# Kernel tuning notes

Measured on AMD Instinct MI355X. Metric: run time of the kernel, lower is better.

## Reference

```python
import jax, jax.numpy as jnp
import numpy as np

B, F, U, A, H = 8192, 1024, 256, 16, 8  # batch, in_features, units_layer, num_actions, hidden(=8)


def _coagent_layer(x, W0, b0, W1, b1, W2, b2):
    # x: [B, f_in]; stacked weights for U independent tiny MLPs (grouped GEMMs)
    h = jax.nn.relu(jnp.einsum('bf,uhf->buh', x, W0) + b0)   # [B, U, H]
    h = jax.nn.relu(jnp.einsum('buh,ugh->bug', h, W1) + b1)  # [B, U, H]
    q = jnp.einsum('bug,uag->bua', h, W2) + b2               # [B, U, A]
    # greedy action per coagent (epsilon-greedy with greedy=True / epsilon=0)
    return jnp.argmax(q, axis=-1).astype(jnp.float32)        # [B, U]


def setup_inputs() -> dict:
    key = jax.random.key(0)
    ks = jax.random.split(key, 19)
    n = lambda k, shape, fan: (jax.random.normal(k, shape, dtype=jnp.float32)
                               / jnp.sqrt(jnp.float32(fan)))
    return {
        'state': jax.random.normal(ks[0], (B, F), dtype=jnp.float32),
        # coagent layer 0: in_features -> 8 -> 8 -> A, stacked over U units
        'W0_0': n(ks[1], (U, H, F), F), 'b0_0': jnp.zeros((U, H), jnp.float32),
        'W1_0': n(ks[2], (U, H, H), H), 'b1_0': jnp.zeros((U, H), jnp.float32),
        'W2_0': n(ks[3], (U, A, H), H), 'b2_0': jnp.zeros((U, A), jnp.float32),
        # coagent layer 1: units_layer -> 8 -> 8 -> A, stacked over U units
        'W0_1': n(ks[4], (U, H, U), U), 'b0_1': jnp.zeros((U, H), jnp.float32),
        'W1_1': n(ks[5], (U, H, H), H), 'b1_1': jnp.zeros((U, H), jnp.float32),
        'W2_1': n(ks[6], (U, A, H), H), 'b2_1': jnp.zeros((U, A), jnp.float32),
        # Policy head: units_layer -> 8 -> 8 -> 1
        'PW0': n(ks[7], (H, U), U), 'Pb0': jnp.zeros((H,), jnp.float32),
        'PW1': n(ks[8], (H, H), H), 'Pb1': jnp.zeros((H,), jnp.float32),
        'PW2': n(ks[9], (1, H), H), 'Pb2': jnp.zeros((1,), jnp.float32),
    }


def reference(state, W0_0, b0_0, W1_0, b1_0, W2_0, b2_0,
              W0_1, b0_1, W1_1, b1_1, W2_1, b2_1,
              PW0, Pb0, PW1, Pb1, PW2, Pb2):
    a0 = _coagent_layer(state, W0_0, b0_0, W1_0, b1_0, W2_0, b2_0)  # [B, U]
    a1 = _coagent_layer(a0, W0_1, b0_1, W1_1, b1_1, W2_1, b2_1)     # [B, U]
    h = jax.nn.relu(a1 @ PW0.T + Pb0)
    h = jax.nn.relu(h @ PW1.T + Pb1)
    return h @ PW2.T + Pb2  # [B, 1]
```

## Files before the change

kernel.cpp:

```cpp
#include <hip/hip_runtime.h>
#include <cstring>
#include <cstdint>

#define B_TOTAL 8192
#define F_IN    1024
#define U_UNITS 256
#define NACT    16
#define HID     8

typedef float    f32x4  __attribute__((ext_vector_type(4)));
typedef _Float16 half8  __attribute__((ext_vector_type(8)));


__device__ __forceinline__ void gload_lds16(const _Float16* g, _Float16* l)
{
    __builtin_amdgcn_global_load_lds(
        (const __attribute__((address_space(1))) void*)g,
        (__attribute__((address_space(3))) void*)l,
        16, 0, 0);
}

__global__ __launch_bounds__(256)
void pack3_kernel(const float* __restrict__ s0, _Float16* __restrict__ d0h, _Float16* __restrict__ d0l,
                  const float* __restrict__ s1, _Float16* __restrict__ d1h, _Float16* __restrict__ d1l,
                  const float* __restrict__ s2, _Float16* __restrict__ d2h, _Float16* __restrict__ d2l)
{
    constexpr int NB0 = (B_TOTAL / 16) * (F_IN / 128);
    constexpr int NB1 = (U_UNITS * HID / 16) * (F_IN / 128);
    __shared__ float ls[16 * 132];
    int b = blockIdx.x;
    const float* src; _Float16 *dh, *dl; int K, lg;
    if (b < NB0)            { src = s0; dh = d0h; dl = d0l; K = F_IN;    lg = 3; }
    else if (b < NB0 + NB1) { b -= NB0; src = s1; dh = d1h; dl = d1l; K = F_IN; lg = 3; }
    else                    { b -= NB0 + NB1; src = s2; dh = d2h; dl = d2l; K = U_UNITS; lg = 1; }

    const int tid = threadIdx.x;
    const int mt  = b >> lg;
    const int kb  = b & ((1 << lg) - 1);
    const int r0  = mt * 16;

#pragma unroll
    for (int i = 0; i < 2; ++i) {
        const int e = tid + (i << 8);
        const int row = e >> 5;
        const int c4  = e & 31;
        f32x4 v = *reinterpret_cast<const f32x4*>(
            &src[(size_t)(r0 + row) * K + (kb << 7) + (c4 << 2)]);
        *reinterpret_cast<f32x4*>(&ls[row * 132 + (c4 << 2)]) = v;
    }
    __syncthreads();

    const int k8 = tid >> 4, r = tid & 15;
    float x[8];
#pragma unroll
    for (int j = 0; j < 8; ++j) x[j] = ls[r * 132 + (k8 << 3) + j];
    half8 h, l;
#pragma unroll
    for (int j = 0; j < 8; ++j) {
        h[j] = (_Float16)x[j];
        l[j] = (_Float16)((x[j] - (float)h[j]) * 2048.0f);
    }
    const size_t off = (((size_t)mt * (K >> 5)) + (kb << 2) + (k8 >> 2)) * 512
                     + (size_t)(((k8 & 3) << 4) + r) * 8;
    *reinterpret_cast<half8*>(&dh[off]) = h;
    *reinterpret_cast<half8*>(&dl[off]) = l;
}

constexpr int BM = 128, BN = 64;

template<int K_TOTAL, bool A_SPLIT, bool OUT_TF32>
__global__ __launch_bounds__(256, 4)
void coagent_mfma(const _Float16* __restrict__ Ahg, const _Float16* __restrict__ Alg,
                  const _Float16* __restrict__ Bhg, const _Float16* __restrict__ Blg,
                  const float* __restrict__ b0, const float* __restrict__ W1,
                  const float* __restrict__ b1, const float* __restrict__ W2,
                  const float* __restrict__ b2, void* __restrict__ outp)
{
    constexpr int BUFH  = A_SPLIT ? 12288 : 8192;
    constexpr int BOFFH = A_SPLIT ? 8192 : 4096;
    constexpr int BOFFL = A_SPLIT ? 10240 : 6144;
    constexpr int NCH   = A_SPLIT ? 6 : 4;

    struct EpiBufs { float Hs[BM][BN + 1]; _Float16 ab[BM * 8]; };
    union SMemU { _Float16 stage[2][BUFH]; EpiBufs epi; };
    __shared__ SMemU sm;

    constexpr int NTK = K_TOTAL >> 5;
    constexpr size_t TS = (size_t)NTK * 512;

    const int tid  = threadIdx.x;
    const int wave = tid >> 6;
    const int lane = tid & 63;
    const int quad = lane >> 4;
    const int l15  = lane & 15;

    const int m0 = blockIdx.y * BM;
    const int n0 = blockIdx.x * BN;

    const int wmi = wave >> 1, wni = wave & 1;
    const int at  = wmi * 4;
    const int bt  = wni * 2;
    const int wm  = wmi * 64, wn = wni * 32;

    const _Float16* gs[NCH];
#pragma unroll
    for (int i = 0; i < NCH; ++i) {
        const int c = wave * NCH + i;
        const _Float16* base; int tile;
        if (A_SPLIT) {
            if (c < 8)       { base = Ahg; tile = (m0 >> 4) + c; }
            else if (c < 16) { base = Alg; tile = (m0 >> 4) + (c - 8); }
            else if (c < 20) { base = Bhg; tile = (n0 >> 4) + (c - 16); }
            else             { base = Blg; tile = (n0 >> 4) + (c - 20); }
        } else {
            if (c < 8)       { base = Ahg; tile = (m0 >> 4) + c; }
            else if (c < 12) { base = Bhg; tile = (n0 >> 4) + (c - 8); }
            else             { base = Blg; tile = (n0 >> 4) + (c - 12); }
        }
        gs[i] = base + (size_t)tile * TS + lane * 8;
    }

    f32x4 acc1[4][2];
    f32x4 acc2[4][2];
#pragma unroll
    for (int i = 0; i < 4; ++i)
#pragma unroll
        for (int j = 0; j < 2; ++j) { acc1[i][j] = {0.f,0.f,0.f,0.f}; acc2[i][j] = {0.f,0.f,0.f,0.f}; }

#pragma unroll
    for (int i = 0; i < NCH; ++i)
        gload_lds16(gs[i], &sm.stage[0][(wave * NCH + i) * 512]);
    __syncthreads();

    int cur = 0;
#pragma unroll 1
    for (int kt = 0; kt < NTK; ++kt) {
        if (kt + 1 < NTK) {
            _Float16* nb = &sm.stage[cur ^ 1][0];
#pragma unroll
            for (int i = 0; i < NCH; ++i)
                gload_lds16(gs[i] + (size_t)(kt + 1) * 512, nb + (wave * NCH + i) * 512);
        }

        const _Float16* sb = &sm.stage[cur][0];
        half8 af[4], la[4];
#pragma unroll
        for (int mt = 0; mt < 4; ++mt)
            af[mt] = *reinterpret_cast<const half8*>(&sb[(at + mt) * 512 + lane * 8]);
        if constexpr (A_SPLIT) {
#pragma unroll
            for (int mt = 0; mt < 4; ++mt)
                la[mt] = *reinterpret_cast<const half8*>(&sb[4096 + (at + mt) * 512 + lane * 8]);
        }

#pragma unroll
        for (int nt = 0; nt < 2; ++nt) {
            half8 bf = *reinterpret_cast<const half8*>(&sb[BOFFH + (bt + nt) * 512 + lane * 8]);
            half8 lb = *reinterpret_cast<const half8*>(&sb[BOFFL + (bt + nt) * 512 + lane * 8]);
#pragma unroll
            for (int mt = 0; mt < 4; ++mt)
                acc1[mt][nt] = __builtin_amdgcn_mfma_f32_16x16x32_f16(af[mt], bf, acc1[mt][nt], 0, 0, 0);
            if constexpr (A_SPLIT) {
#pragma unroll
                for (int mt = 0; mt < 4; ++mt)
                    acc2[mt][nt] = __builtin_amdgcn_mfma_f32_16x16x32_f16(la[mt], bf, acc2[mt][nt], 0, 0, 0);
            }
#pragma unroll
            for (int mt = 0; mt < 4; ++mt)
                acc2[mt][nt] = __builtin_amdgcn_mfma_f32_16x16x32_f16(af[mt], lb, acc2[mt][nt], 0, 0, 0);
        }

        __syncthreads();
        cur ^= 1;
    }

#pragma unroll
    for (int mt = 0; mt < 4; ++mt)
#pragma unroll
        for (int nt = 0; nt < 2; ++nt)
#pragma unroll
            for (int r = 0; r < 4; ++r)
                sm.epi.Hs[wm + mt * 16 + quad * 4 + r][wn + nt * 16 + l15] =
                    acc1[mt][nt][r] + acc2[mt][nt][r] * (1.0f / 2048.0f);
    __syncthreads();

    const int ubase = n0 >> 3;
#pragma unroll
    for (int p = 0; p < 4; ++p) {
        const int idx = (p << 8) + tid;
        const int ul = idx >> 7;
        const int bl = idx & 127;
        const int u  = __builtin_amdgcn_readfirstlane(ubase + ul);
        const float* __restrict__ b0u = b0 + u * 8;
        const float* __restrict__ W1u = W1 + u * 64;
        const float* __restrict__ b1u = b1 + u * 8;
        const float* __restrict__ W2u = W2 + u * 128;
        const float* __restrict__ b2u = b2 + u * 16;

        float h[HID];
#pragma unroll
        for (int j = 0; j < HID; ++j)
            h[j] = fmaxf(sm.epi.Hs[bl][ul * 8 + j] + b0u[j], 0.f);

        float h2[HID];
#pragma unroll
        for (int g = 0; g < HID; ++g) {
            float s = b1u[g];
#pragma unroll
            for (int j = 0; j < HID; ++j)
                s += h[j] * W1u[g * 8 + j];
            h2[g] = fmaxf(s, 0.f);
        }

        float best = b2u[0];
#pragma unroll
        for (int j = 0; j < HID; ++j) best += h2[j] * W2u[j];
        int bi = 0;
#pragma unroll
        for (int a = 1; a < NACT; ++a) {
            float s = b2u[a];
#pragma unroll
            for (int j = 0; j < HID; ++j)
                s += h2[j] * W2u[a * 8 + j];
            if (s > best) { best = s; bi = a; }
        }

        if (OUT_TF32) {
            ((float*)outp)[(size_t)u * B_TOTAL + m0 + bl] = (float)bi;
        } else {
            sm.epi.ab[bl * 8 + ul] = (_Float16)bi;
        }
    }
    if (!OUT_TF32) {
        __syncthreads();
        if (tid < 128) {
            float4 v = *reinterpret_cast<float4*>(&sm.epi.ab[tid * 8]);
            const int u = ubase;
            const int b = m0 + tid;
            const size_t off = ((size_t)(b >> 4) * 8 + (u >> 5)) * 512
                             + (size_t)((((u >> 3) & 3) << 4) + (b & 15)) * 8;
            *reinterpret_cast<float4*>(&((_Float16*)outp)[off]) = v;
        }
    }
}


constexpr int FBM = 128, FBN = 128, FBK = 16;

template<int K_TOTAL, bool X_TRANSPOSED>
__global__ __launch_bounds__(256, 2)
void coagent_kernel(const float* __restrict__ X, const float* __restrict__ W0,
                    const float* __restrict__ b0, const float* __restrict__ W1,
                    const float* __restrict__ b1, const float* __restrict__ W2,
                    const float* __restrict__ b2, float* __restrict__ outT)
{
    struct SMemGemm { float As[FBK][FBM + 4]; float Bs[FBK][FBN + 4]; };
    union SMem { SMemGemm g; float Hs[FBM][65]; };
    __shared__ SMem sm;

    const int tid = threadIdx.x;
    const int tx = tid & 15, ty = tid >> 4;
    const int m0 = blockIdx.y * FBM, n0 = blockIdx.x * FBN;

    float acc[8][8];
#pragma unroll
    for (int i = 0; i < 8; ++i)
#pragma unroll
        for (int j = 0; j < 8; ++j) acc[i][j] = 0.f;

    for (int k0 = 0; k0 < K_TOTAL; k0 += FBK) {
        __syncthreads();
        if (X_TRANSPOSED) {
#pragma unroll
            for (int l = tid; l < (FBM * FBK) / 4; l += 256) {
                const int k = l >> 5, q = l & 31;
                const float4 v = *reinterpret_cast<const float4*>(
                    &X[(size_t)(k0 + k) * B_TOTAL + m0 + 4 * q]);
                *reinterpret_cast<float4*>(&sm.g.As[k][4 * q]) = v;
            }
        } else {
#pragma unroll
            for (int l = tid; l < (FBM * FBK) / 4; l += 256) {
                const int row = l >> 2, c = l & 3;
                const float4 v = *reinterpret_cast<const float4*>(
                    &X[(size_t)(m0 + row) * K_TOTAL + k0 + 4 * c]);
                sm.g.As[4 * c + 0][row] = v.x; sm.g.As[4 * c + 1][row] = v.y;
                sm.g.As[4 * c + 2][row] = v.z; sm.g.As[4 * c + 3][row] = v.w;
            }
        }
#pragma unroll
        for (int l = tid; l < (FBN * FBK) / 4; l += 256) {
            const int row = l >> 2, c = l & 3;
            const float4 v = *reinterpret_cast<const float4*>(
                &W0[(size_t)(n0 + row) * K_TOTAL + k0 + 4 * c]);
            sm.g.Bs[4 * c + 0][row] = v.x; sm.g.Bs[4 * c + 1][row] = v.y;
            sm.g.Bs[4 * c + 2][row] = v.z; sm.g.Bs[4 * c + 3][row] = v.w;
        }
        __syncthreads();
#pragma unroll
        for (int k = 0; k < FBK; ++k) {
            float a[8], bb[8];
            *reinterpret_cast<float4*>(&a[0])  = *reinterpret_cast<float4*>(&sm.g.As[k][4 * ty]);
            *reinterpret_cast<float4*>(&a[4])  = *reinterpret_cast<float4*>(&sm.g.As[k][64 + 4 * ty]);
            *reinterpret_cast<float4*>(&bb[0]) = *reinterpret_cast<float4*>(&sm.g.Bs[k][4 * tx]);
            *reinterpret_cast<float4*>(&bb[4]) = *reinterpret_cast<float4*>(&sm.g.Bs[k][64 + 4 * tx]);
#pragma unroll
            for (int i = 0; i < 8; ++i)
#pragma unroll
                for (int j = 0; j < 8; ++j) acc[i][j] += a[i] * bb[j];
        }
    }

    const int ub_base = n0 >> 3;
    for (int half = 0; half < 2; ++half) {
        __syncthreads();
#pragma unroll
        for (int i = 0; i < 8; ++i) {
            const int row = (i < 4) ? (4 * ty + i) : (64 + 4 * ty + (i - 4));
#pragma unroll
            for (int j = 0; j < 4; ++j)
                sm.Hs[row][4 * tx + j] = acc[i][4 * half + j];
        }
        __syncthreads();
#pragma unroll
        for (int p = 0; p < 4; ++p) {
            const int pair = (p << 8) + tid;
            const int ul = pair >> 7, bl = pair & 127;
            const int u = ub_base + half * 8 + ul;
            float h[HID];
#pragma unroll
            for (int j = 0; j < HID; ++j)
                h[j] = fmaxf(sm.Hs[bl][ul * 8 + j] + b0[u * 8 + j], 0.f);
            float h2[HID];
#pragma unroll
            for (int g = 0; g < HID; ++g) {
                float s = b1[u * 8 + g];
#pragma unroll
                for (int j = 0; j < HID; ++j) s += h[j] * W1[u * 64 + g * 8 + j];
                h2[g] = fmaxf(s, 0.f);
            }
            float best = b2[u * 16];
#pragma unroll
            for (int j = 0; j < HID; ++j) best += h2[j] * W2[u * 128 + j];
            int bi = 0;
#pragma unroll
            for (int a = 1; a < NACT; ++a) {
                float s = b2[u * 16 + a];
#pragma unroll
                for (int j = 0; j < HID; ++j) s += h2[j] * W2[u * 128 + a * 8 + j];
                if (s > best) { best = s; bi = a; }
            }
            outT[(size_t)u * B_TOTAL + m0 + bl] = (float)bi;
        }
    }
}

__global__ __launch_bounds__(256)
void policy_kernel(const float* __restrict__ A1T,
                   const float* __restrict__ PW0, const float* __restrict__ Pb0,
                   const float* __restrict__ PW1, const float* __restrict__ Pb1,
                   const float* __restrict__ PW2, const float* __restrict__ Pb2,
                   float* __restrict__ out)
{
    __shared__ float part[8][32][HID + 1];
    const int tid = threadIdx.x;
    const int b32 = tid & 31;
    const int sl  = tid >> 5;
    const int b   = blockIdx.x * 32 + b32;

    float hp[HID];
#pragma unroll
    for (int j = 0; j < HID; ++j) hp[j] = 0.f;

#pragma unroll 1
    for (int q0 = 0; q0 < 32; q0 += 8) {
        float v[8];
#pragma unroll
        for (int t = 0; t < 8; ++t)
            v[t] = A1T[(size_t)(sl * 32 + q0 + t) * B_TOTAL + b];
#pragma unroll
        for (int t = 0; t < 8; ++t)
#pragma unroll
            for (int j = 0; j < HID; ++j)
                hp[j] += v[t] * PW0[j * U_UNITS + sl * 32 + q0 + t];
    }
#pragma unroll
    for (int j = 0; j < HID; ++j) part[sl][b32][j] = hp[j];
    __syncthreads();

    if (sl == 0) {
        float h[HID];
#pragma unroll
        for (int j = 0; j < HID; ++j) {
            float s = Pb0[j];
#pragma unroll
            for (int s8 = 0; s8 < 8; ++s8) s += part[s8][b32][j];
            h[j] = fmaxf(s, 0.f);
        }
        float h2[HID];
#pragma unroll
        for (int g = 0; g < HID; ++g) {
            float s = Pb1[g];
#pragma unroll
            for (int j = 0; j < HID; ++j) s += h[j] * PW1[g * 8 + j];
            h2[g] = fmaxf(s, 0.f);
        }
        float o = Pb2[0];
#pragma unroll
        for (int j = 0; j < HID; ++j) o += h2[j] * PW2[j];
        out[b] = o;
    }
}


extern "C" void kernel_launch(void* const* d_in, const int* in_sizes, int n_in,
                              void* d_out, int out_size, void* d_ws, size_t ws_size,
                              hipStream_t stream)
{
    const float* state = (const float*)d_in[0];
    const float* W0_0  = (const float*)d_in[1];
    const float* b0_0  = (const float*)d_in[2];
    const float* W1_0  = (const float*)d_in[3];
    const float* b1_0  = (const float*)d_in[4];
    const float* W2_0  = (const float*)d_in[5];
    const float* b2_0  = (const float*)d_in[6];
    const float* W0_1  = (const float*)d_in[7];
    const float* b0_1  = (const float*)d_in[8];
    const float* W1_1  = (const float*)d_in[9];
    const float* b1_1  = (const float*)d_in[10];
    const float* W2_1  = (const float*)d_in[11];
    const float* b2_1  = (const float*)d_in[12];
    const float* PW0   = (const float*)d_in[13];
    const float* Pb0   = (const float*)d_in[14];
    const float* PW1   = (const float*)d_in[15];
    const float* Pb1   = (const float*)d_in[16];
    const float* PW2   = (const float*)d_in[17];
    const float* Pb2   = (const float*)d_in[18];

    const size_t SZ_STATE = (size_t)B_TOTAL * F_IN;
    const size_t SZ_W00   = (size_t)U_UNITS * HID * F_IN;
    const size_t SZ_W01   = (size_t)U_UNITS * HID * U_UNITS;
    const size_t NEED = (2 * SZ_STATE + 2 * SZ_W00 + 2 * SZ_W01
                         + (size_t)B_TOTAL * U_UNITS) * 2
                        + (size_t)U_UNITS * B_TOTAL * 4;

    if (ws_size >= NEED) {
        char* p = (char*)d_ws;
        _Float16* state_h = (_Float16*)p;                p += SZ_STATE * 2;
        _Float16* state_l = (_Float16*)p;                p += SZ_STATE * 2;
        _Float16* w00_h   = (_Float16*)p;                p += SZ_W00 * 2;
        _Float16* w00_l   = (_Float16*)p;                p += SZ_W00 * 2;
        _Float16* w01_h   = (_Float16*)p;                p += SZ_W01 * 2;
        _Float16* w01_l   = (_Float16*)p;                p += SZ_W01 * 2;
        _Float16* a0      = (_Float16*)p;                p += (size_t)B_TOTAL * U_UNITS * 2;
        float*    a1T     = (float*)p;

        constexpr int NB0 = (B_TOTAL / 16) * (F_IN / 128);
        constexpr int NB1 = (U_UNITS * HID / 16) * (F_IN / 128);
        constexpr int NB2 = (U_UNITS * HID / 16) * (U_UNITS / 128);
        pack3_kernel<<<NB0 + NB1 + NB2, 256, 0, stream>>>(
            state, state_h, state_l, W0_0, w00_h, w00_l, W0_1, w01_h, w01_l);

        dim3 grid((U_UNITS * HID) / BN, B_TOTAL / BM);

        coagent_mfma<F_IN, true, false><<<grid, 256, 0, stream>>>(
            state_h, state_l, w00_h, w00_l, b0_0, W1_0, b1_0, W2_0, b2_0, (void*)a0);

        coagent_mfma<U_UNITS, false, true><<<grid, 256, 0, stream>>>(
            a0, nullptr, w01_h, w01_l, b0_1, W1_1, b1_1, W2_1, b2_1, (void*)a1T);

        policy_kernel<<<B_TOTAL / 32, 256, 0, stream>>>(
            a1T, PW0, Pb0, PW1, Pb1, PW2, Pb2, (float*)d_out);
    } else {
        float* a0T = (float*)d_ws;
        float* a1T = a0T + (size_t)U_UNITS * B_TOTAL;
        dim3 grid((U_UNITS * HID) / FBN, B_TOTAL / FBM);
        coagent_kernel<F_IN, false><<<grid, 256, 0, stream>>>(
            state, W0_0, b0_0, W1_0, b1_0, W2_0, b2_0, a0T);
        coagent_kernel<U_UNITS, true><<<grid, 256, 0, stream>>>(
            a0T, W0_1, b0_1, W1_1, b1_1, W2_1, b2_1, a1T);
        policy_kernel<<<B_TOTAL / 32, 256, 0, stream>>>(
            a1T, PW0, Pb0, PW1, Pb1, PW2, Pb2, (float*)d_out);
    }
}
```

Baseline: 281.9 us.

## Triple-buffer LDS staging with prefetch distance two and explicit vmcnt waits

The K loop moves from double to triple buffering in LDS. Global-to-LDS loads are now issued two tiles ahead, and explicit s_waitcnt vmcnt counts wait only for the current tile, so one raw barrier per iteration replaces the trailing __syncthreads. The goal is to hide more global load latency behind the MFMA work and cut barrier stalls. In exchange, LDS use grows and the launch bounds lower the blocks-per-CU target to 2 or 3, which trades occupancy for deeper in-flight prefetch.

```diff
diff --git a/kernel.cpp b/kernel.cpp
--- a/kernel.cpp
+++ b/kernel.cpp
@@ -69,7 +69,7 @@
 constexpr int BM = 128, BN = 64;
 
 template<int K_TOTAL, bool A_SPLIT, bool OUT_TF32>
-__global__ __launch_bounds__(256, 4)
+__global__ __launch_bounds__(256, A_SPLIT ? 2 : 3)
 void coagent_mfma(const _Float16* __restrict__ Ahg, const _Float16* __restrict__ Alg,
                   const _Float16* __restrict__ Bhg, const _Float16* __restrict__ Blg,
                   const float* __restrict__ b0, const float* __restrict__ W1,
@@ -82,7 +82,7 @@
     constexpr int NCH   = A_SPLIT ? 6 : 4;
 
     struct EpiBufs { float Hs[BM][BN + 1]; _Float16 ab[BM * 8]; };
-    union SMemU { _Float16 stage[2][BUFH]; EpiBufs epi; };
+    union SMemU { _Float16 stage[3][BUFH]; EpiBufs epi; };
     __shared__ SMemU sm;
 
     constexpr int NTK = K_TOTAL >> 5;
@@ -102,10 +102,11 @@
     const int bt  = wni * 2;
     const int wm  = wmi * 64, wn = wni * 32;
 
+    const int wave_u = __builtin_amdgcn_readfirstlane(wave);
     const _Float16* gs[NCH];
 #pragma unroll
     for (int i = 0; i < NCH; ++i) {
-        const int c = wave * NCH + i;
+        const int c = wave_u * NCH + i;
         const _Float16* base; int tile;
         if (A_SPLIT) {
             if (c < 8)       { base = Ahg; tile = (m0 >> 4) + c; }
@@ -117,8 +118,9 @@
             else if (c < 12) { base = Bhg; tile = (n0 >> 4) + (c - 8); }
             else             { base = Blg; tile = (n0 >> 4) + (c - 12); }
         }
-        gs[i] = base + (size_t)tile * TS + lane * 8;
-    }
+        gs[i] = base + (size_t)tile * TS;
+    }
+    const int loff = lane * 8;
 
     f32x4 acc1[4][2];
     f32x4 acc2[4][2];
@@ -129,20 +131,32 @@
 
 #pragma unroll
     for (int i = 0; i < NCH; ++i)
-        gload_lds16(gs[i], &sm.stage[0][(wave * NCH + i) * 512]);
-    __syncthreads();
-
-    int cur = 0;
+        gload_lds16(gs[i] + loff, &sm.stage[0][(wave_u * NCH + i) * 512]);
+#pragma unroll
+    for (int i = 0; i < NCH; ++i)
+        gload_lds16(gs[i] + 512 + loff, &sm.stage[1][(wave_u * NCH + i) * 512]);
+
+    int br = 0, bw = 2;
 #pragma unroll 1
     for (int kt = 0; kt < NTK; ++kt) {
         if (kt + 1 < NTK) {
-            _Float16* nb = &sm.stage[cur ^ 1][0];
+            if constexpr (A_SPLIT) asm volatile("s_waitcnt vmcnt(6)" ::: "memory");
+            else                   asm volatile("s_waitcnt vmcnt(4)" ::: "memory");
+        } else {
+            asm volatile("s_waitcnt vmcnt(0)" ::: "memory");
+        }
+        __builtin_amdgcn_s_barrier();
+        __builtin_amdgcn_sched_barrier(0);
+
+        if (kt + 2 < NTK) {
+            _Float16* nb = &sm.stage[bw][0];
 #pragma unroll
             for (int i = 0; i < NCH; ++i)
-                gload_lds16(gs[i] + (size_t)(kt + 1) * 512, nb + (wave * NCH + i) * 512);
-        }
-
-        const _Float16* sb = &sm.stage[cur][0];
+                gload_lds16(gs[i] + (size_t)(kt + 2) * 512 + loff,
+                            nb + (wave_u * NCH + i) * 512);
+        }
+
+        const _Float16* sb = &sm.stage[br][0];
         half8 af[4], la[4];
 #pragma unroll
         for (int mt = 0; mt < 4; ++mt)
@@ -170,9 +184,10 @@
                 acc2[mt][nt] = __builtin_amdgcn_mfma_f32_16x16x32_f16(af[mt], lb, acc2[mt][nt], 0, 0, 0);
         }
 
-        __syncthreads();
-        cur ^= 1;
-    }
+        br = (br == 2) ? 0 : br + 1;
+        bw = (bw == 2) ? 0 : bw + 1;
+    }
+    __syncthreads();
 
 #pragma unroll
     for (int mt = 0; mt < 4; ++mt)
```

After: 283.2 us. Within noise of the previous version (+0.4%).
